# Kernel optimization log

Hardware: AMD Instinct MI355X
Metric: run time of the kernel (lower is better)

The kernel has to match this reference:

```python
import jax, jax.numpy as jnp
import numpy as np
from jax import lax

# The 4 fixed 3x3 Sobel/diagonal kernels used by edge_conv2d128.
_SOBELS = jnp.asarray(np.stack([
    np.array([[-1, 0, 1], [-2, 0, 2], [-1, 0, 1]], dtype=np.float32),
    np.array([[ 1, 2, 1], [ 0, 0, 0], [-1,-2,-1]], dtype=np.float32),
    np.array([[ 2, 1, 0], [ 1, 0,-1], [ 0,-1,-2]], dtype=np.float32),
    np.array([[ 0,-1,-2], [ 1, 0,-1], [ 2, 1, 0]], dtype=np.float32),
], axis=0))  # [4, 3, 3]


def _edge_conv(x):
    """Faithful math of edge_conv2d128: 4 convs whose CxCx3x3 weights are the
    same Sobel kernel tiled over all in/out channels, abs each branch, sum.

    Because every (out_ch, in_ch) weight slice is identical, the tiled conv
    equals conv(sum_over_channels(x), sobel) broadcast to all C output
    channels -- we exploit that structure (identical math, one channel sum
    plus a single 4-output-channel 3x3 conv).
    """
    s = jnp.sum(x, axis=1, keepdims=True)              # [B, 1, H, W]
    k = _SOBELS[:, None, :, :]                          # [4, 1, 3, 3] OIHW
    e = lax.conv_general_dilated(
        s, k, window_strides=(1, 1), padding='SAME',
        dimension_numbers=('NCHW', 'OIHW', 'NCHW'))     # [B, 4, H, W]
    edge = jnp.sum(jnp.abs(e), axis=1, keepdims=True)   # [B, 1, H, W]
    return jnp.broadcast_to(edge, x.shape)              # [B, C, H, W]


def _maxpool2x2(x):
    # nn.MaxPool2d(kernel_size=2, stride=2)
    return lax.reduce_window(
        x, -jnp.inf, lax.max,
        window_dimensions=(1, 1, 2, 2),
        window_strides=(1, 1, 2, 2),
        padding='VALID')


def setup_inputs() -> dict:
    key = jax.random.key(0)
    x = jax.random.normal(key, (2, 128, 512, 512), dtype=jnp.float32)
    return {"x": x}


def reference(x) -> jnp.ndarray:
    # edge_conv2d128 (4 tiled Sobel convs + abs + sum) fused with downsample()
    return _maxpool2x2(_edge_conv(x))  # [B, C, H/2, W/2]
```

## Files before the change

kernel.cpp:

```cpp
#include <hip/hip_runtime.h>
#include <hip/hip_bf16.h>
#include <math.h>


#define N 2
#define C 128
#define H 512
#define W 512
#define HW (H * W)
#define PH 256
#define PW 256
#define PHW (PH * PW)

__global__ void __launch_bounds__(256) ksum_channels(const float* __restrict__ x,
                                                     float* __restrict__ s) {
    int idx = blockIdx.x * blockDim.x + threadIdx.x;
    const int per_n = HW / 4;
    int n  = idx / per_n;
    int sp = idx % per_n;
    const float4* xp = (const float4*)(x + (size_t)n * C * HW) + sp;
    float4 acc = make_float4(0.f, 0.f, 0.f, 0.f);
#pragma unroll 8
    for (int c = 0; c < C; ++c) {
        float4 v = xp[(size_t)c * per_n];
        acc.x += v.x; acc.y += v.y; acc.z += v.z; acc.w += v.w;
    }
    ((float4*)s)[idx] = acc;
}

__global__ void __launch_bounds__(256) kedge_pool_bcast(const float* __restrict__ s,
                                                        float* __restrict__ out) {
    int idx = blockIdx.x * blockDim.x + threadIdx.x;
    const int per_n = PH * (PW / 4);
    int n   = idx / per_n;
    int r   = idx % per_n;
    int ph  = r / (PW / 4);
    int pw4 = (r % (PW / 4)) * 4;

    const float* sp = s + (size_t)n * HW;

    const int r0 = 2 * ph - 1;
    const int c0 = 2 * pw4 - 1;
    float v[4][10];
#pragma unroll
    for (int i = 0; i < 4; ++i) {
        int rr = r0 + i;
        bool rok = (rr >= 0) && (rr < H);
#pragma unroll
        for (int j = 0; j < 10; ++j) {
            int cc = c0 + j;
            bool ok = rok && (cc >= 0) && (cc < W);
            v[i][j] = ok ? sp[(size_t)rr * W + cc] : 0.f;
        }
    }

    float pool[4];
#pragma unroll
    for (int q = 0; q < 4; ++q) {
        float m = 0.f;
#pragma unroll
        for (int a = 0; a < 2; ++a) {
#pragma unroll
            for (int b = 0; b < 2; ++b) {
                int jb = 2 * q + b;
                float p00 = v[a    ][jb], p01 = v[a    ][jb + 1], p02 = v[a    ][jb + 2];
                float p10 = v[a + 1][jb], p11 = v[a + 1][jb + 1], p12 = v[a + 1][jb + 2];
                float p20 = v[a + 2][jb], p21 = v[a + 2][jb + 1], p22 = v[a + 2][jb + 2];
                (void)p11;
                float e0 = -p00 + p02 - 2.f * p10 + 2.f * p12 - p20 + p22;
                float e1 =  p00 + 2.f * p01 + p02 - p20 - 2.f * p21 - p22;
                float e2 = 2.f * p00 + p01 + p10 - p12 - p21 - 2.f * p22;
                float e3 = -p01 - 2.f * p02 + p10 - p12 + 2.f * p20 + p21;
                float edge = fabsf(e0) + fabsf(e1) + fabsf(e2) + fabsf(e3);
                m = fmaxf(m, edge);
            }
        }
        pool[q] = m;
    }
    float4 pv = make_float4(pool[0], pool[1], pool[2], pool[3]);

    int cbase = blockIdx.y * 16;
    size_t base = (size_t)n * C * PHW + (size_t)cbase * PHW + (size_t)ph * PW + pw4;
#pragma unroll
    for (int c = 0; c < 16; ++c) {
        *(float4*)(out + base + (size_t)c * PHW) = pv;
    }
}

extern "C" void kernel_launch(void* const* d_in, const int* in_sizes, int n_in,
                              void* d_out, int out_size, void* d_ws, size_t ws_size,
                              hipStream_t stream) {
    const float* x = (const float*)d_in[0];
    float* out = (float*)d_out;
    float* s   = (float*)d_ws;

    ksum_channels<<<dim3((N * HW / 4) / 256), dim3(256), 0, stream>>>(x, s);

    kedge_pool_bcast<<<dim3((N * PH * (PW / 4)) / 256, 8), dim3(256), 0, stream>>>(s, out);
}
```

Baseline: 387.4 us.

## Split channel sum into partial groups and use zero-padded sum plane

The channel reduction is split into 4 groups of 32 channels, each writing its own partial-sum plane. A reduce kernel then adds the partials into a zero-padded plane, which lets the edge/pool kernel load its stencil without bounds checks. The aim is four times more parallelism in the bandwidth-bound read of the 268MB input, since the original launched only 512 blocks. The cost is an extra memset, an extra kernel launch, and an extra 8MB of partial-sum traffic.

```diff
diff --git a/kernel.cpp b/kernel.cpp
--- a/kernel.cpp
+++ b/kernel.cpp
@@ -12,47 +12,64 @@
 #define PW 256
 #define PHW (PH * PW)
 
-__global__ void __launch_bounds__(256) ksum_channels(const float* __restrict__ x,
-                                                     float* __restrict__ s) {
+#define NHW4 (N * HW / 4)
+#define SW 520
+#define SR 514
+#define SPLANE (SR * SW)
+
+__global__ void __launch_bounds__(256) ksum_partial(const float* __restrict__ x,
+                                                    float* __restrict__ part) {
     int idx = blockIdx.x * blockDim.x + threadIdx.x;
-    const int per_n = HW / 4;
-    int n  = idx / per_n;
-    int sp = idx % per_n;
-    const float4* xp = (const float4*)(x + (size_t)n * C * HW) + sp;
+    int g   = blockIdx.y;
+    int n   = idx >> 16;
+    int sp  = idx & 65535;
+    const float4* xp = (const float4*)(x + (size_t)n * C * HW) +
+                       (size_t)g * 32 * (HW / 4) + sp;
     float4 acc = make_float4(0.f, 0.f, 0.f, 0.f);
 #pragma unroll 8
-    for (int c = 0; c < C; ++c) {
-        float4 v = xp[(size_t)c * per_n];
+    for (int c = 0; c < 32; ++c) {
+        float4 v = xp[(size_t)c * (HW / 4)];
         acc.x += v.x; acc.y += v.y; acc.z += v.z; acc.w += v.w;
     }
-    ((float4*)s)[idx] = acc;
+    ((float4*)part)[(size_t)g * NHW4 + idx] = acc;
 }
 
-__global__ void __launch_bounds__(256) kedge_pool_bcast(const float* __restrict__ s,
+__global__ void __launch_bounds__(256) kreduce_pad(const float* __restrict__ part,
+                                                   float* __restrict__ spad) {
+    int idx = blockIdx.x * blockDim.x + threadIdx.x;
+    int n  = idx >> 16;
+    int sp = idx & 65535;
+    int r  = sp / (W / 4);
+    int c4 = (sp % (W / 4)) * 4;
+    const float4* p = (const float4*)part;
+    float4 a = p[idx];
+    float4 b = p[idx + NHW4];
+    float4 c = p[idx + 2 * NHW4];
+    float4 d = p[idx + 3 * NHW4];
+    float4 s;
+    s.x = (a.x + b.x) + (c.x + d.x);
+    s.y = (a.y + b.y) + (c.y + d.y);
+    s.z = (a.z + b.z) + (c.z + d.z);
+    s.w = (a.w + b.w) + (c.w + d.w);
+    *(float4*)(spad + (size_t)n * SPLANE + (size_t)(r + 1) * SW + (c4 + 4)) = s;
+}
+
+__global__ void __launch_bounds__(256) kedge_pool_bcast(const float* __restrict__ spad,
                                                         float* __restrict__ out) {
     int idx = blockIdx.x * blockDim.x + threadIdx.x;
-    const int per_n = PH * (PW / 4);
-    int n   = idx / per_n;
-    int r   = idx % per_n;
+    int n   = idx / (PH * (PW / 4));
+    int r   = idx % (PH * (PW / 4));
     int ph  = r / (PW / 4);
     int pw4 = (r % (PW / 4)) * 4;
 
-    const float* sp = s + (size_t)n * HW;
+    const float* sp = spad + (size_t)n * SPLANE + (size_t)(2 * ph) * SW + (2 * pw4 + 3);
 
-    const int r0 = 2 * ph - 1;
-    const int c0 = 2 * pw4 - 1;
     float v[4][10];
 #pragma unroll
-    for (int i = 0; i < 4; ++i) {
-        int rr = r0 + i;
-        bool rok = (rr >= 0) && (rr < H);
+    for (int i = 0; i < 4; ++i)
 #pragma unroll
-        for (int j = 0; j < 10; ++j) {
-            int cc = c0 + j;
-            bool ok = rok && (cc >= 0) && (cc < W);
-            v[i][j] = ok ? sp[(size_t)rr * W + cc] : 0.f;
-        }
-    }
+        for (int j = 0; j < 10; ++j)
+            v[i][j] = sp[(size_t)i * SW + j];
 
     float pool[4];
 #pragma unroll
@@ -64,9 +81,8 @@
             for (int b = 0; b < 2; ++b) {
                 int jb = 2 * q + b;
                 float p00 = v[a    ][jb], p01 = v[a    ][jb + 1], p02 = v[a    ][jb + 2];
-                float p10 = v[a + 1][jb], p11 = v[a + 1][jb + 1], p12 = v[a + 1][jb + 2];
+                float p10 = v[a + 1][jb],                         p12 = v[a + 1][jb + 2];
                 float p20 = v[a + 2][jb], p21 = v[a + 2][jb + 1], p22 = v[a + 2][jb + 2];
-                (void)p11;
                 float e0 = -p00 + p02 - 2.f * p10 + 2.f * p12 - p20 + p22;
                 float e1 =  p00 + 2.f * p01 + p02 - p20 - 2.f * p21 - p22;
                 float e2 = 2.f * p00 + p01 + p10 - p12 - p21 - 2.f * p22;
@@ -82,19 +98,23 @@
     int cbase = blockIdx.y * 16;
     size_t base = (size_t)n * C * PHW + (size_t)cbase * PHW + (size_t)ph * PW + pw4;
 #pragma unroll
-    for (int c = 0; c < 16; ++c) {
+    for (int c = 0; c < 16; ++c)
         *(float4*)(out + base + (size_t)c * PHW) = pv;
-    }
 }
 
 extern "C" void kernel_launch(void* const* d_in, const int* in_sizes, int n_in,
                               void* d_out, int out_size, void* d_ws, size_t ws_size,
                               hipStream_t stream) {
     const float* x = (const float*)d_in[0];
-    float* out = (float*)d_out;
-    float* s   = (float*)d_ws;
+    float* out  = (float*)d_out;
+    float* part = (float*)d_ws;
+    float* spad = (float*)((char*)d_ws + (size_t)8 * 1024 * 1024);
 
-    ksum_channels<<<dim3((N * HW / 4) / 256), dim3(256), 0, stream>>>(x, s);
+    hipMemsetAsync(spad, 0, (size_t)N * SPLANE * sizeof(float), stream);
 
-    kedge_pool_bcast<<<dim3((N * PH * (PW / 4)) / 256, 8), dim3(256), 0, stream>>>(s, out);
+    ksum_partial<<<dim3(NHW4 / 256, 4), dim3(256), 0, stream>>>(x, part);
+
+    kreduce_pad<<<dim3(NHW4 / 256), dim3(256), 0, stream>>>(part, spad);
+
+    kedge_pool_bcast<<<dim3((N * PH * (PW / 4)) / 256, 8), dim3(256), 0, stream>>>(spad, out);
 }
```

New measurement: 380.0 us. About the same (-1.9%).
